# Performance work log

Measured on AMD Instinct MI355X. Metric: run time of the kernel, lower is better.

## Reference

```python
import jax, jax.numpy as jnp
import numpy as np

B, T, H, S, P, NH, NL = 16, 4096, 1024, 16, 6, 8, 2
EPS = 1e-5

def _ln(x, g, b):
    m = x.mean(-1, keepdims=True)
    v = ((x - m) ** 2).mean(-1, keepdims=True)
    return (x - m) / jnp.sqrt(v + EPS) * g + b

def _mha(q, k, v, in_w, in_b, out_w, out_b, kpm):
    dh = H // NH
    wq, wk, wv = jnp.split(in_w, 3, axis=0)
    bq, bk, bv = jnp.split(in_b, 3, axis=0)
    qh = (q @ wq.T + bq).reshape(q.shape[0], q.shape[1], NH, dh)
    kh = (k @ wk.T + bk).reshape(k.shape[0], k.shape[1], NH, dh)
    vh = (v @ wv.T + bv).reshape(v.shape[0], v.shape[1], NH, dh)
    sc = jnp.einsum('bqhd,bkhd->bhqk', qh, kh) / np.float32(np.sqrt(dh))
    if kpm is not None:
        sc = jnp.where(kpm[:, None, None, :], -1e30, sc)
    a = jax.nn.softmax(sc, axis=-1)
    o = jnp.einsum('bhqk,bkhd->bqhd', a, vh).reshape(q.shape[0], q.shape[1], H)
    return o @ out_w.T + out_b

def _segment_pool(hidden, mask):
    # vectorized ragged per-segment mean over the valid prefix of each sequence
    L = mask.sum(-1)  # [B] valid lengths (assumed >= S)
    s = jnp.arange(S + 1, dtype=jnp.float32)
    bounds = jnp.floor(s[None, :] * L[:, None].astype(jnp.float32) / S).astype(jnp.int32)  # [B,S+1]
    pos = jnp.arange(T)
    valid = pos[None, :] < L[:, None]  # [B,T]
    seg_id = (pos[None, :, None] >= bounds[:, None, 1:S]).sum(-1)  # [B,T] in [0,S-1]
    oh = ((seg_id[:, :, None] == jnp.arange(S)) & valid[:, :, None]).astype(hidden.dtype)  # [B,T,S]
    seg_sum = jnp.einsum('bts,bth->bsh', oh, hidden)
    cnt = oh.sum(1)  # [B,S]
    seg_states = seg_sum / jnp.maximum(cnt, 1.0)[..., None]
    return seg_states, cnt > 0

def setup_inputs() -> dict:
    key = jax.random.key(0)
    ks = jax.random.split(key, 32)
    p = lambda k, shp: (jax.random.normal(k, shp, jnp.float32) * 0.02)
    token_states = jax.random.normal(ks[0], (B, T, H), jnp.float32)
    lengths = jax.random.randint(ks[1], (B,), T // 2, T + 1)
    attention_mask = (jnp.arange(T)[None, :] < lengths[:, None]).astype(jnp.int32)
    inp = dict(
        token_states=token_states, attention_mask=attention_mask,
        sa_in_w=p(ks[2], (3 * H, H)), sa_in_b=jnp.zeros((3 * H,)),
        sa_out_w=p(ks[3], (H, H)), sa_out_b=jnp.zeros((H,)),
        ln_g=jnp.ones((H,)), ln_b=jnp.zeros((H,)),
        sal_w1=p(ks[4], (H, H)), sal_b1=jnp.zeros((H,)),
        sal_w2=p(ks[5], (1, H)), sal_b2=jnp.zeros((1,)),
        plan_q=p(ks[6], (P, H)),
        qa_in_w=p(ks[7], (3 * H, H)), qa_in_b=jnp.zeros((3 * H,)),
        qa_out_w=p(ks[8], (H, H)), qa_out_b=jnp.zeros((H,)),
        r_in_w=p(ks[9], (NL, 3 * H, H)), r_in_b=jnp.zeros((NL, 3 * H)),
        r_out_w=p(ks[10], (NL, H, H)), r_out_b=jnp.zeros((NL, H)),
        r_ln1_g=jnp.ones((NL, H)), r_ln1_b=jnp.zeros((NL, H)),
        r_ln2_g=jnp.ones((NL, H)), r_ln2_b=jnp.zeros((NL, H)),
        r_w1=p(ks[11], (NL, 4 * H, H)), r_b1=jnp.zeros((NL, 4 * H)),
        r_w2=p(ks[12], (NL, H, 4 * H)), r_b2=jnp.zeros((NL, H)),
    )
    return inp

def reference(token_states, attention_mask, sa_in_w, sa_in_b, sa_out_w, sa_out_b,
              ln_g, ln_b, sal_w1, sal_b1, sal_w2, sal_b2, plan_q,
              qa_in_w, qa_in_b, qa_out_w, qa_out_b,
              r_in_w, r_in_b, r_out_w, r_out_b,
              r_ln1_g, r_ln1_b, r_ln2_g, r_ln2_b, r_w1, r_b1, r_w2, r_b2):
    seg, seg_mask = _segment_pool(token_states, attention_mask)
    kpm = ~seg_mask
    attn = _mha(seg, seg, seg, sa_in_w, sa_in_b, sa_out_w, sa_out_b, kpm)
    seg = _ln(seg + attn, ln_g, ln_b)
    h = jax.nn.gelu(seg @ sal_w1.T + sal_b1, approximate=False)
    logits = (h @ sal_w2.T + sal_b2)[..., 0]
    logits = jnp.where(seg_mask, logits, -10000.0)
    sal = jax.nn.softmax(logits, axis=-1)
    wseg = seg * sal[..., None]
    query = jnp.broadcast_to(plan_q[None], (token_states.shape[0], P, H))
    plan = _mha(query, wseg, wseg, qa_in_w, qa_in_b, qa_out_w, qa_out_b, kpm)
    for l in range(NL):  # norm_first TransformerEncoder layers
        y = _ln(plan, r_ln1_g[l], r_ln1_b[l])
        plan = plan + _mha(y, y, y, r_in_w[l], r_in_b[l], r_out_w[l], r_out_b[l], None)
        y = _ln(plan, r_ln2_g[l], r_ln2_b[l])
        y = jax.nn.gelu(y @ r_w1[l].T + r_b1[l], approximate=False) @ r_w2[l].T + r_b2[l]
        plan = plan + y
    entropy = -(sal * jnp.log(sal + 1e-8)).sum(-1).mean()
    nrm = jnp.maximum(jnp.linalg.norm(plan, axis=-1, keepdims=True), 1e-12)
    npn = plan / nrm
    sim = jnp.einsum('bph,bqh->bpq', npn, npn)
    off = sim * (1.0 - jnp.eye(P, dtype=sim.dtype))
    redundancy = (off ** 2).sum() / (plan.shape[0] * P * (P - 1))
    return plan, sal, entropy, redundancy
```

## Files before the change

### kernel.cpp

```cpp
#include <hip/hip_runtime.h>
#include <hip/hip_bf16.h>
#include <math.h>

#define BB 16
#define TT 4096
#define HH 1024
#define SS 16
#define PP 6
#define NHH 8
#define DHH 128
#define NLL 2

typedef __hip_bfloat16 bf16;

__device__ __forceinline__ float b2f(bf16 x){ return __bfloat162float(x); }
__device__ __forceinline__ float us2f(unsigned short u){ return __uint_as_float(((unsigned)u) << 16); }

template<int ISBF>
__device__ __forceinline__ float ldw(const void* p, size_t i){
    if (ISBF) return b2f(((const bf16*)p)[i]);
    else      return ((const float*)p)[i];
}

__global__ void k_init(const unsigned* __restrict__ lng, float* __restrict__ scal,
                       int* __restrict__ flag){
    if (threadIdx.x == 0){
        scal[0] = 0.f; scal[1] = 0.f; scal[2] = 0.f; scal[3] = 0.f;
        flag[0] = (lng[0] == 0x3F800000u) ? 0 : 1;
    }
}

__global__ void k_len(const int* __restrict__ mask, int* __restrict__ L){
    int b = blockIdx.x, tid = threadIdx.x;
    int s = 0;
    for (int t = tid; t < TT; t += 256) s += mask[b*TT + t];
    __shared__ int red[256];
    red[tid] = s; __syncthreads();
    for (int w = 128; w > 0; w >>= 1){ if (tid < w) red[tid] += red[tid+w]; __syncthreads(); }
    if (tid == 0) L[b] = red[0];
}

template<int ISBF>
__device__ void segpool_body(const void* __restrict__ tok, const int* __restrict__ L,
                             float* __restrict__ seg){
    int s = blockIdx.x, b = blockIdx.y;
    int len = L[b];
    int lo = (s*len)/SS, hi = ((s+1)*len)/SS;
    int tid = threadIdx.x;
    int h0 = tid*4;
    float a0=0.f,a1=0.f,a2=0.f,a3=0.f;
    if (ISBF){
        const bf16* t = (const bf16*)tok;
        for (int tt = lo; tt < hi; ++tt){
            ushort4 u = *(const ushort4*)(t + ((size_t)(b*TT + tt))*HH + h0);
            a0 += us2f(u.x); a1 += us2f(u.y); a2 += us2f(u.z); a3 += us2f(u.w);
        }
    } else {
        const float* t = (const float*)tok;
        for (int tt = lo; tt < hi; ++tt){
            float4 u = *(const float4*)(t + ((size_t)(b*TT + tt))*HH + h0);
            a0 += u.x; a1 += u.y; a2 += u.z; a3 += u.w;
        }
    }
    float inv = 1.0f/(float)(hi-lo);
    float* o = seg + ((size_t)(b*SS + s))*HH + h0;
    o[0]=a0*inv; o[1]=a1*inv; o[2]=a2*inv; o[3]=a3*inv;
}
__global__ void k_segpool(const void* __restrict__ tok, const int* __restrict__ L,
                          float* __restrict__ seg, const int* __restrict__ flag){
    if (*flag) segpool_body<1>(tok, L, seg); else segpool_body<0>(tok, L, seg);
}

__global__ __launch_bounds__(256) void k_gemmsk(
        const float* __restrict__ X, const void* __restrict__ W,
        float* __restrict__ part, int N, int K, int M,
        size_t offW, int kChunk, const int* __restrict__ flag){
    __shared__ float As[16][68], Bs[16][68];
    const int tid = threadIdx.x;
    const int r0 = blockIdx.y*64, c0 = blockIdx.x*64;
    const int tx = tid & 15, ty = tid >> 4;
    const int sr = tid >> 2;
    const int sk = (tid & 3) << 2;
    const int kbeg = blockIdx.z * kChunk, kend = kbeg + kChunk;
    const int isbf = *flag;
    float c[4][4] = {{0.f,0.f,0.f,0.f},{0.f,0.f,0.f,0.f},{0.f,0.f,0.f,0.f},{0.f,0.f,0.f,0.f}};
    for (int k0 = kbeg; k0 < kend; k0 += 16){
        float4 av = make_float4(0.f,0.f,0.f,0.f);
        if (r0 + sr < N) av = *(const float4*)(X + (size_t)(r0+sr)*K + k0 + sk);
        float4 bv;
        if (isbf){
            ushort4 u = *(const ushort4*)((const bf16*)W + offW + (size_t)(c0+sr)*K + k0 + sk);
            bv = make_float4(us2f(u.x), us2f(u.y), us2f(u.z), us2f(u.w));
        } else {
            bv = *(const float4*)((const float*)W + offW + (size_t)(c0+sr)*K + k0 + sk);
        }
        As[sk+0][sr]=av.x; As[sk+1][sr]=av.y; As[sk+2][sr]=av.z; As[sk+3][sr]=av.w;
        Bs[sk+0][sr]=bv.x; Bs[sk+1][sr]=bv.y; Bs[sk+2][sr]=bv.z; Bs[sk+3][sr]=bv.w;
        __syncthreads();
        #pragma unroll
        for (int kk = 0; kk < 16; ++kk){
            float4 a = *(const float4*)&As[kk][ty<<2];
            float4 b = *(const float4*)&Bs[kk][tx<<2];
            c[0][0] += a.x*b.x; c[0][1] += a.x*b.y; c[0][2] += a.x*b.z; c[0][3] += a.x*b.w;
            c[1][0] += a.y*b.x; c[1][1] += a.y*b.y; c[1][2] += a.y*b.z; c[1][3] += a.y*b.w;
            c[2][0] += a.z*b.x; c[2][1] += a.z*b.y; c[2][2] += a.z*b.z; c[2][3] += a.z*b.w;
            c[3][0] += a.w*b.x; c[3][1] += a.w*b.y; c[3][2] += a.w*b.z; c[3][3] += a.w*b.w;
        }
        __syncthreads();
    }
    float* dst = part + (size_t)blockIdx.z * ((size_t)N * M);
    #pragma unroll
    for (int i = 0; i < 4; ++i){
        int r = r0 + (ty<<2) + i;
        if (r < N){
            float4 st = make_float4(c[i][0], c[i][1], c[i][2], c[i][3]);
            *(float4*)(dst + (size_t)r*M + c0 + (tx<<2)) = st;
        }
    }
}

template<int ACT, int RES>
__global__ void k_epi(const float* __restrict__ part, const void* __restrict__ bias,
                      const float* __restrict__ R, float* __restrict__ Y,
                      int M, int offB, int total, int SK, const int* __restrict__ flag){
    int i = blockIdx.x*256 + threadIdx.x;
    if (i >= total) return;
    float v = 0.f;
    for (int z = 0; z < SK; ++z) v += part[(size_t)z*total + i];
    int col = i % M;
    v += (*flag) ? b2f(((const bf16*)bias)[offB + col]) : ((const float*)bias)[offB + col];
    if (ACT == 1) v = 0.5f*v*(1.0f + erff(v*0.70710678118654752f));
    if (RES == 1) v += R[i];
    Y[i] = v;
}

static void gemm_sk(hipStream_t st, const float* X, const void* W, const void* bias,
                    const float* R, float* Y, float* part, const int* flag,
                    int N, int K, int M, size_t offW, int offB, int SK, int act, int res){
    dim3 g(M/64, (N+63)/64, SK);
    k_gemmsk<<<g, 256, 0, st>>>(X, W, part, N, K, M, offW, K/SK, flag);
    int total = N*M;
    int nb = (total + 255)/256;
    if (act){
        if (res) k_epi<1,1><<<nb,256,0,st>>>(part, bias, R, Y, M, offB, total, SK, flag);
        else     k_epi<1,0><<<nb,256,0,st>>>(part, bias, R, Y, M, offB, total, SK, flag);
    } else {
        if (res) k_epi<0,1><<<nb,256,0,st>>>(part, bias, R, Y, M, offB, total, SK, flag);
        else     k_epi<0,0><<<nb,256,0,st>>>(part, bias, R, Y, M, offB, total, SK, flag);
    }
}

__global__ void k_attn(const float* __restrict__ Qb, const float* __restrict__ Kb,
                       const float* __restrict__ Vb, float* __restrict__ O,
                       int nq, int nk, int sQ, int sKV, int qShared){
    __shared__ float Qs[16][DHH], Ks[16][DHH], Vs[16][DHH];
    __shared__ float sc[16][17];
    int b = blockIdx.x / NHH, h = blockIdx.x % NHH;
    int tid = threadIdx.x;
    for (int idx = tid; idx < nq*DHH; idx += 256){
        int i = idx >> 7, d = idx & 127;
        int r = qShared ? i : (b*nq + i);
        Qs[i][d] = Qb[(size_t)r*sQ + h*DHH + d];
    }
    for (int idx = tid; idx < nk*DHH; idx += 256){
        int j = idx >> 7, d = idx & 127;
        Ks[j][d] = Kb[(size_t)(b*nk + j)*sKV + h*DHH + d];
        Vs[j][d] = Vb[(size_t)(b*nk + j)*sKV + h*DHH + d];
    }
    __syncthreads();
    const float scale = 0.0883883476483184406f;
    for (int idx = tid; idx < nq*nk; idx += 256){
        int i = idx / nk, j = idx % nk;
        float s = 0.f;
        for (int d = 0; d < DHH; ++d) s += Qs[i][d]*Ks[j][d];
        sc[i][j] = s * scale;
    }
    __syncthreads();
    if (tid < nq){
        float m = -1e30f;
        for (int j = 0; j < nk; ++j) m = fmaxf(m, sc[tid][j]);
        float ssum = 0.f;
        for (int j = 0; j < nk; ++j){ float e = expf(sc[tid][j] - m); sc[tid][j] = e; ssum += e; }
        float inv = 1.0f/ssum;
        for (int j = 0; j < nk; ++j) sc[tid][j] *= inv;
    }
    __syncthreads();
    for (int idx = tid; idx < nq*DHH; idx += 256){
        int i = idx >> 7, d = idx & 127;
        float o = 0.f;
        for (int j = 0; j < nk; ++j) o += sc[i][j]*Vs[j][d];
        O[(size_t)(b*nq + i)*HH + h*DHH + d] = o;
    }
}

template<int ISBF>
__device__ void ln_body(const float* __restrict__ X, const void* __restrict__ g,
                        const void* __restrict__ bta, float* __restrict__ Y, int off){
    int row = blockIdx.x, tid = threadIdx.x;
    const float* x = X + (size_t)row*HH;
    float v[4]; float s = 0.f, sq = 0.f;
    #pragma unroll
    for (int u = 0; u < 4; ++u){ v[u] = x[tid + u*256]; s += v[u]; sq += v[u]*v[u]; }
    __shared__ float r1[256], r2[256];
    r1[tid] = s; r2[tid] = sq; __syncthreads();
    for (int w = 128; w > 0; w >>= 1){
        if (tid < w){ r1[tid] += r1[tid+w]; r2[tid] += r2[tid+w]; }
        __syncthreads();
    }
    float mean = r1[0]*(1.0f/HH);
    float var  = fmaxf(r2[0]*(1.0f/HH) - mean*mean, 0.f);
    float rstd = rsqrtf(var + 1e-5f);
    float* y = Y + (size_t)row*HH;
    #pragma unroll
    for (int u = 0; u < 4; ++u){
        int c = tid + u*256;
        y[c] = (v[u]-mean)*rstd*ldw<ISBF>(g, (size_t)(off+c)) + ldw<ISBF>(bta, (size_t)(off+c));
    }
}
__global__ void k_ln(const float* __restrict__ X, const void* __restrict__ g,
                     const void* __restrict__ bta, float* __restrict__ Y,
                     int off, const int* __restrict__ flag){
    if (*flag) ln_body<1>(X,g,bta,Y,off); else ln_body<0>(X,g,bta,Y,off);
}

template<int ISBF>
__device__ void sal_body(const float* __restrict__ Hbuf, const void* __restrict__ w2,
                         const void* __restrict__ b2v, float* __restrict__ sal,
                         float* __restrict__ scal){
    int b = blockIdx.x, tid = threadIdx.x;
    __shared__ float red[256];
    __shared__ float lg[SS];
    for (int s = 0; s < SS; ++s){
        const float* hr = Hbuf + (size_t)(b*SS + s)*HH;
        float acc = 0.f;
        for (int k = tid; k < HH; k += 256) acc += hr[k]*ldw<ISBF>(w2, (size_t)k);
        red[tid] = acc; __syncthreads();
        for (int w = 128; w > 0; w >>= 1){ if (tid < w) red[tid] += red[tid+w]; __syncthreads(); }
        if (tid == 0) lg[s] = red[0] + ldw<ISBF>(b2v, 0);
        __syncthreads();
    }
    if (tid == 0){
        float m = -1e30f;
        for (int s = 0; s < SS; ++s) m = fmaxf(m, lg[s]);
        float ssum = 0.f;
        for (int s = 0; s < SS; ++s){ float e = expf(lg[s]-m); lg[s] = e; ssum += e; }
        float inv = 1.0f/ssum, ent = 0.f;
        for (int s = 0; s < SS; ++s){
            float p = lg[s]*inv;
            sal[b*SS+s] = p;
            ent -= p*logf(p + 1e-8f);
        }
        atomicAdd(&scal[0], ent);
    }
}
__global__ void k_sal(const float* __restrict__ Hbuf, const void* __restrict__ w2,
                      const void* __restrict__ b2v, float* __restrict__ sal,
                      float* __restrict__ scal, const int* __restrict__ flag){
    if (*flag) sal_body<1>(Hbuf,w2,b2v,sal,scal); else sal_body<0>(Hbuf,w2,b2v,sal,scal);
}

__global__ void k_wseg(const float* __restrict__ seg, const float* __restrict__ sal,
                       float* __restrict__ wseg){
    int i = blockIdx.x*256 + threadIdx.x;
    wseg[i] = seg[i]*sal[i/HH];
}

__global__ void k_cvt(const void* __restrict__ in, float* __restrict__ out, int n,
                      const int* __restrict__ flag){
    int i = blockIdx.x*256 + threadIdx.x;
    if (i < n){
        if (*flag) out[i] = b2f(((const bf16*)in)[i]);
        else       out[i] = ((const float*)in)[i];
    }
}

__global__ void k_red(const float* __restrict__ plan, float* __restrict__ scal){
    int b = blockIdx.x, tid = threadIdx.x;
    __shared__ float Pl[PP][HH];
    __shared__ float red[256];
    __shared__ float nrm[PP];
    for (int idx = tid; idx < PP*HH; idx += 256)
        Pl[idx/HH][idx%HH] = plan[(size_t)b*PP*HH + idx];
    __syncthreads();
    for (int p = 0; p < PP; ++p){
        float a = 0.f;
        for (int k = tid; k < HH; k += 256){ float v = Pl[p][k]; a += v*v; }
        red[tid] = a; __syncthreads();
        for (int w = 128; w > 0; w >>= 1){ if (tid < w) red[tid] += red[tid+w]; __syncthreads(); }
        if (tid == 0) nrm[p] = fmaxf(sqrtf(red[0]), 1e-12f);
        __syncthreads();
    }
    float total = 0.f;
    for (int p = 0; p < PP; ++p){
        for (int q = p+1; q < PP; ++q){
            float a = 0.f;
            for (int k = tid; k < HH; k += 256) a += Pl[p][k]*Pl[q][k];
            red[tid] = a; __syncthreads();
            for (int w = 128; w > 0; w >>= 1){ if (tid < w) red[tid] += red[tid+w]; __syncthreads(); }
            if (tid == 0){ float s = red[0]/(nrm[p]*nrm[q]); total += 2.0f*s*s; }
            __syncthreads();
        }
    }
    if (tid == 0) atomicAdd(&scal[1], total);
}

__global__ void k_out(const float* __restrict__ plan, const float* __restrict__ sal,
                      const float* __restrict__ scal, void* __restrict__ outv,
                      const int* __restrict__ flag){
    int i = blockIdx.x*256 + threadIdx.x;
    const int NPLAN = BB*PP*HH;
    const int NSAL  = BB*SS;
    float v;
    if (i < NPLAN) v = plan[i];
    else if (i < NPLAN + NSAL) v = sal[i - NPLAN];
    else if (i == NPLAN + NSAL) v = scal[0] * (1.0f/BB);
    else if (i == NPLAN + NSAL + 1) v = scal[1] * (1.0f/(BB*PP*(PP-1)));
    else return;
    if (*flag) ((bf16*)outv)[i] = __float2bfloat16(v);
    else       ((float*)outv)[i] = v;
}

extern "C" void kernel_launch(void* const* d_in, const int* in_sizes, int n_in,
                              void* d_out, int out_size, void* d_ws, size_t ws_size,
                              hipStream_t stream) {
    const void* tok      = d_in[0];
    const int*  mask     = (const int*)d_in[1];
    const void* sa_in_w  = d_in[2];
    const void* sa_in_b  = d_in[3];
    const void* sa_out_w = d_in[4];
    const void* sa_out_b = d_in[5];
    const void* ln_g     = d_in[6];
    const void* ln_b     = d_in[7];
    const void* sal_w1   = d_in[8];
    const void* sal_b1   = d_in[9];
    const void* sal_w2   = d_in[10];
    const void* sal_b2   = d_in[11];
    const void* plan_q   = d_in[12];
    const void* qa_in_w  = d_in[13];
    const void* qa_in_b  = d_in[14];
    const void* qa_out_w = d_in[15];
    const void* qa_out_b = d_in[16];
    const void* r_in_w   = d_in[17];
    const void* r_in_b   = d_in[18];
    const void* r_out_w  = d_in[19];
    const void* r_out_b  = d_in[20];
    const void* r_ln1_g  = d_in[21];
    const void* r_ln1_b  = d_in[22];
    const void* r_ln2_g  = d_in[23];
    const void* r_ln2_b  = d_in[24];
    const void* r_w1     = d_in[25];
    const void* r_b1     = d_in[26];
    const void* r_w2     = d_in[27];
    const void* r_b2     = d_in[28];

    float* ws   = (float*)d_ws;
    float* seg  = ws;
    float* qkv  = seg  + BB*SS*HH;
    float* t1   = qkv  + BB*SS*3*HH;
    float* t2   = t1   + BB*SS*HH;
    float* plan = t2   + BB*SS*HH;
    float* ybuf = plan + BB*PP*HH;
    float* qkv2 = ybuf + BB*PP*HH;
    float* pbuf = qkv2 + BB*PP*4*HH;
    float* sal  = pbuf + BB*PP*HH;
    float* qx   = sal  + BB*SS;
    float* qh   = qx   + PP*HH;
    float* part = qh   + PP*HH;
    float* scal = part + 2*BB*SS*3*HH;
    int*   Lw   = (int*)(scal + 4);
    int*   flag = Lw + BB;

    k_init<<<1, 64, 0, stream>>>((const unsigned*)ln_g, scal, flag);
    k_len<<<BB, 256, 0, stream>>>(mask, Lw);
    k_segpool<<<dim3(SS, BB), 256, 0, stream>>>(tok, Lw, seg, flag);

    gemm_sk(stream, seg, sa_in_w, sa_in_b, nullptr, qkv, part, flag,
            BB*SS, HH, 3*HH, (size_t)0, 0, 2, 0, 0);
    k_attn<<<BB*NHH, 256, 0, stream>>>(qkv, qkv+HH, qkv+2*HH, t1, SS, SS, 3*HH, 3*HH, 0);
    gemm_sk(stream, t1, sa_out_w, sa_out_b, seg, t2, part, flag,
            BB*SS, HH, HH, (size_t)0, 0, 4, 0, 1);
    k_ln<<<BB*SS, 256, 0, stream>>>(t2, ln_g, ln_b, seg, 0, flag);

    gemm_sk(stream, seg, sal_w1, sal_b1, nullptr, t1, part, flag,
            BB*SS, HH, HH, (size_t)0, 0, 4, 1, 0);
    k_sal<<<BB, 256, 0, stream>>>(t1, sal_w2, sal_b2, sal, scal, flag);
    k_wseg<<<BB*SS*HH/256, 256, 0, stream>>>(seg, sal, t2);

    k_cvt<<<(PP*HH+255)/256, 256, 0, stream>>>(plan_q, qx, PP*HH, flag);
    gemm_sk(stream, qx, qa_in_w, qa_in_b, nullptr, qh, part, flag,
            PP, HH, HH, (size_t)0, 0, 8, 0, 0);
    gemm_sk(stream, t2, qa_in_w, qa_in_b, nullptr, qkv, part, flag,
            BB*SS, HH, 2*HH, (size_t)HH*HH, HH, 2, 0, 0);
    k_attn<<<BB*NHH, 256, 0, stream>>>(qh, qkv, qkv+HH, pbuf, PP, SS, HH, 2*HH, 1);
    gemm_sk(stream, pbuf, qa_out_w, qa_out_b, nullptr, plan, part, flag,
            BB*PP, HH, HH, (size_t)0, 0, 8, 0, 0);

    for (int l = 0; l < NLL; ++l){
        k_ln<<<BB*PP, 256, 0, stream>>>(plan, r_ln1_g, r_ln1_b, ybuf, l*HH, flag);
        gemm_sk(stream, ybuf, r_in_w, r_in_b, nullptr, qkv2, part, flag,
                BB*PP, HH, 3*HH, (size_t)l*3*HH*HH, l*3*HH, 4, 0, 0);
        k_attn<<<BB*NHH, 256, 0, stream>>>(qkv2, qkv2+HH, qkv2+2*HH, pbuf, PP, PP, 3*HH, 3*HH, 0);
        gemm_sk(stream, pbuf, r_out_w, r_out_b, plan, plan, part, flag,
                BB*PP, HH, HH, (size_t)l*HH*HH, l*HH, 8, 0, 1);
        k_ln<<<BB*PP, 256, 0, stream>>>(plan, r_ln2_g, r_ln2_b, ybuf, l*HH, flag);
        gemm_sk(stream, ybuf, r_w1, r_b1, nullptr, qkv2, part, flag,
                BB*PP, HH, 4*HH, (size_t)l*4*HH*HH, l*4*HH, 2, 1, 0);
        gemm_sk(stream, qkv2, r_w2, r_b2, plan, plan, part, flag,
                BB*PP, 4*HH, HH, (size_t)l*HH*4*HH, l*HH, 8, 0, 1);
    }

    k_red<<<BB, 256, 0, stream>>>(plan, scal);
    k_out<<<(BB*PP*HH + BB*SS + 2 + 255)/256, 256, 0, stream>>>(plan, sal, scal, d_out, flag);
}
```

Measured before the change: 1.039 ms.

## Rewrite pipeline with bf16 MFMA GEMMs, split-precision activations, fused LN and segpool

Replaces the FP32 split-K SIMT GEMMs and their separate epilogue kernels with bf16 MFMA GEMMs. Activations are split into hi/lo bf16 pairs to keep near-fp32 accuracy, and bias, GELU and residual are fused into the GEMM epilogue. Output projections are fused with the following LayerNorm. The length, init and segment-pool kernels are merged into one wider pooling kernel, and the dtype flag is read inline. This cuts launch count, partial-sum traffic and scalar FMA work, at the cost of extra shadow buffers and doubled MFMA count for the lo parts.

```diff
diff --git a/kernel.cpp b/kernel.cpp
--- a/kernel.cpp
+++ b/kernel.cpp
@@ -12,312 +12,608 @@
 #define NLL 2
 
 typedef __hip_bfloat16 bf16;
+typedef __attribute__((ext_vector_type(8))) short s8v;
+typedef __attribute__((ext_vector_type(4))) float f32x4;
+#define MFMA_B16(a,b,c) __builtin_amdgcn_mfma_f32_16x16x32_bf16((a),(b),(c),0,0,0)
 
 __device__ __forceinline__ float b2f(bf16 x){ return __bfloat162float(x); }
 __device__ __forceinline__ float us2f(unsigned short u){ return __uint_as_float(((unsigned)u) << 16); }
-
+__device__ __forceinline__ int is_bf(const unsigned* lng){ return lng[0]==0x3F800000u ? 0 : 1; }
+__device__ __forceinline__ float geluf(float v){ return 0.5f*v*(1.0f+erff(v*0.70710678118654752f)); }
+
+__device__ __forceinline__ void split_bf(float x, ushort& h, ushort& l){
+    unsigned xb = __float_as_uint(x);
+    unsigned hh = (xb + 0x7FFFu + ((xb>>16)&1u)) >> 16;
+    float hf = __uint_as_float(hh<<16);
+    float r = x - hf;
+    unsigned rb = __float_as_uint(r);
+    unsigned ll = (rb + 0x7FFFu + ((rb>>16)&1u)) >> 16;
+    h=(ushort)hh; l=(ushort)ll;
+}
 template<int ISBF>
 __device__ __forceinline__ float ldw(const void* p, size_t i){
     if (ISBF) return b2f(((const bf16*)p)[i]);
     else      return ((const float*)p)[i];
 }
 
-__global__ void k_init(const unsigned* __restrict__ lng, float* __restrict__ scal,
-                       int* __restrict__ flag){
-    if (threadIdx.x == 0){
-        scal[0] = 0.f; scal[1] = 0.f; scal[2] = 0.f; scal[3] = 0.f;
-        flag[0] = (lng[0] == 0x3F800000u) ? 0 : 1;
-    }
-}
-
-__global__ void k_len(const int* __restrict__ mask, int* __restrict__ L){
-    int b = blockIdx.x, tid = threadIdx.x;
-    int s = 0;
-    for (int t = tid; t < TT; t += 256) s += mask[b*TT + t];
-    __shared__ int red[256];
-    red[tid] = s; __syncthreads();
-    for (int w = 128; w > 0; w >>= 1){ if (tid < w) red[tid] += red[tid+w]; __syncthreads(); }
-    if (tid == 0) L[b] = red[0];
-}
-
-template<int ISBF>
-__device__ void segpool_body(const void* __restrict__ tok, const int* __restrict__ L,
-                             float* __restrict__ seg){
-    int s = blockIdx.x, b = blockIdx.y;
-    int len = L[b];
-    int lo = (s*len)/SS, hi = ((s+1)*len)/SS;
-    int tid = threadIdx.x;
-    int h0 = tid*4;
-    float a0=0.f,a1=0.f,a2=0.f,a3=0.f;
-    if (ISBF){
-        const bf16* t = (const bf16*)tok;
-        for (int tt = lo; tt < hi; ++tt){
-            ushort4 u = *(const ushort4*)(t + ((size_t)(b*TT + tt))*HH + h0);
-            a0 += us2f(u.x); a1 += us2f(u.y); a2 += us2f(u.z); a3 += us2f(u.w);
+__global__ __launch_bounds__(1024) void k_segpool(const void* __restrict__ tok,
+        const int* __restrict__ mask, float* __restrict__ seg,
+        ushort* __restrict__ sh, ushort* __restrict__ sl,
+        float* __restrict__ scal, const unsigned* __restrict__ lng){
+    __shared__ float sm[8*1024];
+    int s = blockIdx.x, b = blockIdx.y, tid = threadIdx.x;
+    if (s==0 && b==0 && tid==0){ scal[0]=0.f; scal[1]=0.f; scal[2]=0.f; scal[3]=0.f; }
+    int* smi = (int*)sm;
+    int a0i = 0;
+    #pragma unroll
+    for (int u=0;u<4;++u) a0i += mask[b*TT + tid + u*1024];
+    smi[tid]=a0i; __syncthreads();
+    for (int w=512;w>0;w>>=1){ if (tid<w) smi[tid]+=smi[tid+w]; __syncthreads(); }
+    int len = smi[0];
+    __syncthreads();
+    int lo=(s*len)/SS, hi=((s+1)*len)/SS;
+    float inv = 1.0f/(float)(hi-lo);
+    if (is_bf(lng)){
+        int ro = tid >> 7;
+        int c8 = (tid & 127) << 3;
+        float a[8];
+        #pragma unroll
+        for (int i=0;i<8;++i) a[i]=0.f;
+        const unsigned short* t = (const unsigned short*)tok;
+        for (int tt = lo + ro; tt < hi; tt += 8){
+            uint4 u = *(const uint4*)(t + ((size_t)(b*TT + tt))*HH + c8);
+            a[0]+=us2f((unsigned short)(u.x&0xffff)); a[1]+=us2f((unsigned short)(u.x>>16));
+            a[2]+=us2f((unsigned short)(u.y&0xffff)); a[3]+=us2f((unsigned short)(u.y>>16));
+            a[4]+=us2f((unsigned short)(u.z&0xffff)); a[5]+=us2f((unsigned short)(u.z>>16));
+            a[6]+=us2f((unsigned short)(u.w&0xffff)); a[7]+=us2f((unsigned short)(u.w>>16));
+        }
+        #pragma unroll
+        for (int i=0;i<8;++i) sm[ro*1024 + c8 + i] = a[i];
+        __syncthreads();
+        if (ro == 0){
+            #pragma unroll
+            for (int r=1;r<8;++r)
+                #pragma unroll
+                for (int i=0;i<8;++i) a[i] += sm[r*1024 + c8 + i];
+            size_t base = ((size_t)(b*SS + s))*HH + c8;
+            #pragma unroll
+            for (int i=0;i<8;++i){
+                float v = a[i]*inv;
+                seg[base+i] = v;
+                ushort h_,l_; split_bf(v,h_,l_);
+                sh[base+i]=h_; sl[base+i]=l_;
+            }
         }
     } else {
+        int ro = tid >> 8;
+        int c4 = (tid & 255) << 2;
+        float a[4] = {0.f,0.f,0.f,0.f};
         const float* t = (const float*)tok;
-        for (int tt = lo; tt < hi; ++tt){
-            float4 u = *(const float4*)(t + ((size_t)(b*TT + tt))*HH + h0);
-            a0 += u.x; a1 += u.y; a2 += u.z; a3 += u.w;
-        }
-    }
-    float inv = 1.0f/(float)(hi-lo);
-    float* o = seg + ((size_t)(b*SS + s))*HH + h0;
-    o[0]=a0*inv; o[1]=a1*inv; o[2]=a2*inv; o[3]=a3*inv;
-}
-__global__ void k_segpool(const void* __restrict__ tok, const int* __restrict__ L,
-                          float* __restrict__ seg, const int* __restrict__ flag){
-    if (*flag) segpool_body<1>(tok, L, seg); else segpool_body<0>(tok, L, seg);
-}
-
-__global__ __launch_bounds__(256) void k_gemmsk(
-        const float* __restrict__ X, const void* __restrict__ W,
-        float* __restrict__ part, int N, int K, int M,
-        size_t offW, int kChunk, const int* __restrict__ flag){
+        for (int tt = lo + ro; tt < hi; tt += 4){
+            float4 u = *(const float4*)(t + ((size_t)(b*TT + tt))*HH + c4);
+            a[0]+=u.x; a[1]+=u.y; a[2]+=u.z; a[3]+=u.w;
+        }
+        #pragma unroll
+        for (int i=0;i<4;++i) sm[ro*1024 + c4 + i] = a[i];
+        __syncthreads();
+        if (ro == 0){
+            #pragma unroll
+            for (int r=1;r<4;++r)
+                #pragma unroll
+                for (int i=0;i<4;++i) a[i] += sm[r*1024 + c4 + i];
+            size_t base = ((size_t)(b*SS + s))*HH + c4;
+            #pragma unroll
+            for (int i=0;i<4;++i) seg[base+i] = a[i]*inv;
+        }
+    }
+}
+
+template<int ACT,int RES,int SHAD,int RAWA>
+__global__ __launch_bounds__(256) void k_gemm_t(
+        const float* __restrict__ Xf, const ushort* __restrict__ Ah, const ushort* __restrict__ Al,
+        const void* __restrict__ W, const void* __restrict__ bias, const float* __restrict__ Rres,
+        float* __restrict__ Y, ushort* __restrict__ Yh, ushort* __restrict__ Yl,
+        int N, int K, int M, size_t offW, int offB, const unsigned* __restrict__ lng){
     __shared__ float As[16][68], Bs[16][68];
     const int tid = threadIdx.x;
-    const int r0 = blockIdx.y*64, c0 = blockIdx.x*64;
-    const int tx = tid & 15, ty = tid >> 4;
-    const int sr = tid >> 2;
-    const int sk = (tid & 3) << 2;
-    const int kbeg = blockIdx.z * kChunk, kend = kbeg + kChunk;
-    const int isbf = *flag;
-    float c[4][4] = {{0.f,0.f,0.f,0.f},{0.f,0.f,0.f,0.f},{0.f,0.f,0.f,0.f},{0.f,0.f,0.f,0.f}};
-    for (int k0 = kbeg; k0 < kend; k0 += 16){
-        float4 av = make_float4(0.f,0.f,0.f,0.f);
-        if (r0 + sr < N) av = *(const float4*)(X + (size_t)(r0+sr)*K + k0 + sk);
-        float4 bv;
-        if (isbf){
-            ushort4 u = *(const ushort4*)((const bf16*)W + offW + (size_t)(c0+sr)*K + k0 + sk);
-            bv = make_float4(us2f(u.x), us2f(u.y), us2f(u.z), us2f(u.w));
-        } else {
-            bv = *(const float4*)((const float*)W + offW + (size_t)(c0+sr)*K + k0 + sk);
-        }
-        As[sk+0][sr]=av.x; As[sk+1][sr]=av.y; As[sk+2][sr]=av.z; As[sk+3][sr]=av.w;
-        Bs[sk+0][sr]=bv.x; Bs[sk+1][sr]=bv.y; Bs[sk+2][sr]=bv.z; Bs[sk+3][sr]=bv.w;
-        __syncthreads();
-        #pragma unroll
-        for (int kk = 0; kk < 16; ++kk){
-            float4 a = *(const float4*)&As[kk][ty<<2];
-            float4 b = *(const float4*)&Bs[kk][tx<<2];
-            c[0][0] += a.x*b.x; c[0][1] += a.x*b.y; c[0][2] += a.x*b.z; c[0][3] += a.x*b.w;
-            c[1][0] += a.y*b.x; c[1][1] += a.y*b.y; c[1][2] += a.y*b.z; c[1][3] += a.y*b.w;
-            c[2][0] += a.z*b.x; c[2][1] += a.z*b.y; c[2][2] += a.z*b.z; c[2][3] += a.z*b.w;
-            c[3][0] += a.w*b.x; c[3][1] += a.w*b.y; c[3][2] += a.w*b.z; c[3][3] += a.w*b.w;
-        }
-        __syncthreads();
-    }
-    float* dst = part + (size_t)blockIdx.z * ((size_t)N * M);
-    #pragma unroll
-    for (int i = 0; i < 4; ++i){
-        int r = r0 + (ty<<2) + i;
-        if (r < N){
-            float4 st = make_float4(c[i][0], c[i][1], c[i][2], c[i][3]);
-            *(float4*)(dst + (size_t)r*M + c0 + (tx<<2)) = st;
-        }
-    }
-}
-
-template<int ACT, int RES>
-__global__ void k_epi(const float* __restrict__ part, const void* __restrict__ bias,
-                      const float* __restrict__ R, float* __restrict__ Y,
-                      int M, int offB, int total, int SK, const int* __restrict__ flag){
-    int i = blockIdx.x*256 + threadIdx.x;
-    if (i >= total) return;
-    float v = 0.f;
-    for (int z = 0; z < SK; ++z) v += part[(size_t)z*total + i];
-    int col = i % M;
-    v += (*flag) ? b2f(((const bf16*)bias)[offB + col]) : ((const float*)bias)[offB + col];
-    if (ACT == 1) v = 0.5f*v*(1.0f + erff(v*0.70710678118654752f));
-    if (RES == 1) v += R[i];
-    Y[i] = v;
-}
-
-static void gemm_sk(hipStream_t st, const float* X, const void* W, const void* bias,
-                    const float* R, float* Y, float* part, const int* flag,
-                    int N, int K, int M, size_t offW, int offB, int SK, int act, int res){
-    dim3 g(M/64, (N+63)/64, SK);
-    k_gemmsk<<<g, 256, 0, st>>>(X, W, part, N, K, M, offW, K/SK, flag);
-    int total = N*M;
-    int nb = (total + 255)/256;
-    if (act){
-        if (res) k_epi<1,1><<<nb,256,0,st>>>(part, bias, R, Y, M, offB, total, SK, flag);
-        else     k_epi<1,0><<<nb,256,0,st>>>(part, bias, R, Y, M, offB, total, SK, flag);
+    const int c0 = blockIdx.x*64;
+    if (is_bf(lng)){
+        const int l=tid&63, wv=tid>>6, lr=l&15, lk=(l>>4)<<3;
+        const int r0 = blockIdx.y*64 + wv*16;
+        int ar = r0 + lr; if (ar > N-1) ar = N-1;
+        const ushort* pah = Ah + (size_t)ar*K + lk;
+        const ushort* pal = nullptr;
+        if (!RAWA) pal = Al + (size_t)ar*K + lk;
+        const ushort* pw = (const ushort*)W + offW + (size_t)(c0+lr)*K + lk;
+        const size_t w16 = (size_t)16*K;
+        f32x4 a0={0.f,0.f,0.f,0.f}, a1={0.f,0.f,0.f,0.f};
+        f32x4 a2={0.f,0.f,0.f,0.f}, a3={0.f,0.f,0.f,0.f};
+        for (int k=0;k<K;k+=32){
+            s8v ah = *(const s8v*)pah;
+            s8v b0 = *(const s8v*)pw;
+            s8v b1 = *(const s8v*)(pw + w16);
+            s8v b2 = *(const s8v*)(pw + 2*w16);
+            s8v b3 = *(const s8v*)(pw + 3*w16);
+            a0=MFMA_B16(ah,b0,a0); a1=MFMA_B16(ah,b1,a1);
+            a2=MFMA_B16(ah,b2,a2); a3=MFMA_B16(ah,b3,a3);
+            if (!RAWA){
+                s8v al_ = *(const s8v*)pal;
+                a0=MFMA_B16(al_,b0,a0); a1=MFMA_B16(al_,b1,a1);
+                a2=MFMA_B16(al_,b2,a2); a3=MFMA_B16(al_,b3,a3);
+                pal += 32;
+            }
+            pah += 32; pw += 32;
+        }
+        const int rb = r0 + ((l>>4)<<2);
+        #pragma unroll
+        for (int rg=0;rg<4;++rg){
+            int r = rb+rg;
+            if (r < N){
+                float vv[4] = {a0[rg],a1[rg],a2[rg],a3[rg]};
+                #pragma unroll
+                for (int j=0;j<4;++j){
+                    int col = c0 + j*16 + lr;
+                    float v = vv[j] + ldw<1>(bias,(size_t)(offB+col));
+                    if (ACT) v = geluf(v);
+                    if (RES) v += Rres[(size_t)r*M+col];
+                    Y[(size_t)r*M+col] = v;
+                    if (SHAD){ ushort h_,l_; split_bf(v,h_,l_);
+                        Yh[(size_t)r*M+col]=h_; Yl[(size_t)r*M+col]=l_; }
+                }
+            }
+        }
     } else {
-        if (res) k_epi<0,1><<<nb,256,0,st>>>(part, bias, R, Y, M, offB, total, SK, flag);
-        else     k_epi<0,0><<<nb,256,0,st>>>(part, bias, R, Y, M, offB, total, SK, flag);
-    }
-}
-
-__global__ void k_attn(const float* __restrict__ Qb, const float* __restrict__ Kb,
+        const int r0 = blockIdx.y*64;
+        const int tx = tid&15, ty = tid>>4, sr = tid>>2, sk = (tid&3)<<2;
+        float c4[4][4] = {{0.f,0.f,0.f,0.f},{0.f,0.f,0.f,0.f},{0.f,0.f,0.f,0.f},{0.f,0.f,0.f,0.f}};
+        const float* Xs = RAWA ? Xf : Xf;
+        for (int k0=0;k0<K;k0+=16){
+            float4 av = make_float4(0.f,0.f,0.f,0.f);
+            if (r0+sr < N) av = *(const float4*)(Xs + (size_t)(r0+sr)*K + k0 + sk);
+            float4 bv = *(const float4*)((const float*)W + offW + (size_t)(c0+sr)*K + k0 + sk);
+            As[sk+0][sr]=av.x; As[sk+1][sr]=av.y; As[sk+2][sr]=av.z; As[sk+3][sr]=av.w;
+            Bs[sk+0][sr]=bv.x; Bs[sk+1][sr]=bv.y; Bs[sk+2][sr]=bv.z; Bs[sk+3][sr]=bv.w;
+            __syncthreads();
+            #pragma unroll
+            for (int kk=0;kk<16;++kk){
+                float4 a = *(const float4*)&As[kk][ty<<2];
+                float4 b = *(const float4*)&Bs[kk][tx<<2];
+                c4[0][0]+=a.x*b.x; c4[0][1]+=a.x*b.y; c4[0][2]+=a.x*b.z; c4[0][3]+=a.x*b.w;
+                c4[1][0]+=a.y*b.x; c4[1][1]+=a.y*b.y; c4[1][2]+=a.y*b.z; c4[1][3]+=a.y*b.w;
+                c4[2][0]+=a.z*b.x; c4[2][1]+=a.z*b.y; c4[2][2]+=a.z*b.z; c4[2][3]+=a.z*b.w;
+                c4[3][0]+=a.w*b.x; c4[3][1]+=a.w*b.y; c4[3][2]+=a.w*b.z; c4[3][3]+=a.w*b.w;
+            }
+            __syncthreads();
+        }
+        #pragma unroll
+        for (int i=0;i<4;++i){
+            int r = r0 + (ty<<2) + i;
+            if (r < N){
+                #pragma unroll
+                for (int j=0;j<4;++j){
+                    int col = c0 + (tx<<2) + j;
+                    float v = c4[i][j] + ((const float*)bias)[offB+col];
+                    if (ACT) v = geluf(v);
+                    if (RES) v += Rres[(size_t)r*M+col];
+                    Y[(size_t)r*M+col] = v;
+                }
+            }
+        }
+    }
+}
+
+template<int RES,int HASY>
+__global__ __launch_bounds__(512) void k_rowln(
+        const float* __restrict__ Xf, const ushort* __restrict__ Ah, const ushort* __restrict__ Al,
+        const void* __restrict__ W, const void* __restrict__ bias, const float* __restrict__ Rres,
+        float* __restrict__ Y, float* __restrict__ Z, ushort* __restrict__ Zh, ushort* __restrict__ Zl,
+        const void* __restrict__ g, const void* __restrict__ bta,
+        size_t offW, int offB, int lnoff, const unsigned* __restrict__ lng){
+    __shared__ float smx[8256+320];
+    float* As  = smx;
+    float* smS = smx + 8256;
+    float* smQ = smS + 128;
+    float* smM = smQ + 128;
+    float* smR = smM + 16;
+    const int tid = threadIdx.x;
+    const int r0 = blockIdx.x*16;
+    if (is_bf(lng)){
+        const int w=tid>>6, l=tid&63, lr=l&15, lk=(l>>4)<<3, g4=l>>4;
+        const ushort* pah = Ah + (size_t)(r0+lr)*HH + lk;
+        const ushort* pal = Al + (size_t)(r0+lr)*HH + lk;
+        const int cbase = w*128;
+        const ushort* wp = (const ushort*)W + offW + (size_t)(cbase+lr)*HH + lk;
+        const size_t w16 = (size_t)16*HH;
+        f32x4 acc[8];
+        #pragma unroll
+        for (int s=0;s<8;++s) acc[s] = (f32x4){0.f,0.f,0.f,0.f};
+        for (int k=0;k<HH;k+=32){
+            s8v ah = *(const s8v*)pah;
+            s8v al_ = *(const s8v*)pal;
+            #pragma unroll
+            for (int s=0;s<8;++s){
+                s8v bv = *(const s8v*)(wp + (size_t)s*w16);
+                acc[s]=MFMA_B16(ah,bv,acc[s]);
+                acc[s]=MFMA_B16(al_,bv,acc[s]);
+            }
+            pah+=32; pal+=32; wp+=32;
+        }
+        float ps[4]={0.f,0.f,0.f,0.f}, pq[4]={0.f,0.f,0.f,0.f};
+        #pragma unroll
+        for (int s=0;s<8;++s){
+            int col = cbase + s*16 + lr;
+            float bv = ldw<1>(bias,(size_t)(offB+col));
+            #pragma unroll
+            for (int rg=0;rg<4;++rg){
+                int r = r0 + g4*4 + rg;
+                float v = acc[s][rg] + bv;
+                if (RES)  v += Rres[(size_t)r*HH+col];
+                if (HASY) Y[(size_t)r*HH+col] = v;
+                acc[s][rg] = v;
+                ps[rg]+=v; pq[rg]+=v*v;
+            }
+        }
+        #pragma unroll
+        for (int m=1;m<16;m<<=1){
+            #pragma unroll
+            for (int rg=0;rg<4;++rg){
+                ps[rg]+=__shfl_xor(ps[rg],m);
+                pq[rg]+=__shfl_xor(pq[rg],m);
+            }
+        }
+        if (lr==0){
+            #pragma unroll
+            for (int rg=0;rg<4;++rg){ smS[w*16+g4*4+rg]=ps[rg]; smQ[w*16+g4*4+rg]=pq[rg]; }
+        }
+        __syncthreads();
+        if (tid<16){
+            float S=0.f,Q=0.f;
+            #pragma unroll
+            for (int ww=0;ww<8;++ww){ S+=smS[ww*16+tid]; Q+=smQ[ww*16+tid]; }
+            float mean=S*(1.0f/HH);
+            float var=fmaxf(Q*(1.0f/HH)-mean*mean,0.f);
+            smM[tid]=mean; smR[tid]=rsqrtf(var+1e-5f);
+        }
+        __syncthreads();
+        #pragma unroll
+        for (int s=0;s<8;++s){
+            int col = cbase + s*16 + lr;
+            float gg = ldw<1>(g,(size_t)(lnoff+col));
+            float bb = ldw<1>(bta,(size_t)(lnoff+col));
+            #pragma unroll
+            for (int rg=0;rg<4;++rg){
+                int r = r0 + g4*4 + rg;
+                float zv = (acc[s][rg]-smM[g4*4+rg])*smR[g4*4+rg]*gg+bb;
+                Z[(size_t)r*HH+col]=zv;
+                ushort h_,l_; split_bf(zv,h_,l_);
+                Zh[(size_t)r*HH+col]=h_; Zl[(size_t)r*HH+col]=l_;
+            }
+        }
+    } else {
+        float acc0[16], acc1[16];
+        #pragma unroll
+        for (int r=0;r<16;++r){ acc0[r]=0.f; acc1[r]=0.f; }
+        const float* Wf = (const float*)W;
+        for (int ko=0;ko<HH;ko+=512){
+            for (int i=tid;i<16*512;i+=512){ int rr=i>>9, cc=i&511; As[rr*516+cc]=Xf[(size_t)(r0+rr)*HH+ko+cc]; }
+            __syncthreads();
+            const float* wp0 = Wf + offW + (size_t)tid*HH + ko;
+            const float* wp1 = Wf + offW + (size_t)(tid+512)*HH + ko;
+            for (int k=0;k<512;++k){
+                float wa=wp0[k], wb=wp1[k];
+                #pragma unroll
+                for (int r=0;r<16;++r){ float av=As[r*516+k]; acc0[r]+=av*wa; acc1[r]+=av*wb; }
+            }
+            __syncthreads();
+        }
+        const float* bf_ = (const float*)bias;
+        float b0=bf_[offB+tid], b1v=bf_[offB+tid+512];
+        float s16[16], q16[16];
+        #pragma unroll
+        for (int r=0;r<16;++r){
+            float v0=acc0[r]+b0, v1=acc1[r]+b1v;
+            if (RES){ v0+=Rres[(size_t)(r0+r)*HH+tid]; v1+=Rres[(size_t)(r0+r)*HH+tid+512]; }
+            if (HASY){ Y[(size_t)(r0+r)*HH+tid]=v0; Y[(size_t)(r0+r)*HH+tid+512]=v1; }
+            acc0[r]=v0; acc1[r]=v1;
+            s16[r]=v0+v1; q16[r]=v0*v0+v1*v1;
+        }
+        #pragma unroll
+        for (int m=1;m<64;m<<=1){
+            #pragma unroll
+            for (int r=0;r<16;++r){ s16[r]+=__shfl_xor(s16[r],m); q16[r]+=__shfl_xor(q16[r],m); }
+        }
+        int w=tid>>6, l=tid&63;
+        if (l==0){
+            #pragma unroll
+            for (int r=0;r<16;++r){ smS[w*16+r]=s16[r]; smQ[w*16+r]=q16[r]; }
+        }
+        __syncthreads();
+        if (tid<16){
+            float S=0.f,Q=0.f;
+            #pragma unroll
+            for (int ww=0;ww<8;++ww){ S+=smS[ww*16+tid]; Q+=smQ[ww*16+tid]; }
+            float mean=S*(1.0f/HH);
+            float var=fmaxf(Q*(1.0f/HH)-mean*mean,0.f);
+            smM[tid]=mean; smR[tid]=rsqrtf(var+1e-5f);
+        }
+        __syncthreads();
+        const float* gf=(const float*)g; const float* btf=(const float*)bta;
+        float g0=gf[lnoff+tid], g1=gf[lnoff+tid+512];
+        float t0=btf[lnoff+tid], t1v=btf[lnoff+tid+512];
+        #pragma unroll
+        for (int r=0;r<16;++r){
+            Z[(size_t)(r0+r)*HH+tid]     =(acc0[r]-smM[r])*smR[r]*g0+t0;
+            Z[(size_t)(r0+r)*HH+tid+512] =(acc1[r]-smM[r])*smR[r]*g1+t1v;
+        }
+    }
+}
+
+__global__ __launch_bounds__(512) void k_sal(
+        const float* __restrict__ segF, const ushort* __restrict__ segH, const ushort* __restrict__ segL,
+        const void* __restrict__ w1, const void* __restrict__ b1,
+        const void* __restrict__ w2, const void* __restrict__ b2v,
+        float* __restrict__ sal, float* __restrict__ t2, ushort* __restrict__ t2h, ushort* __restrict__ t2l,
+        float* __restrict__ scal, const unsigned* __restrict__ lng){
+    __shared__ float smx[8256+320];
+    float* As  = smx;
+    float* smS = smx + 8256;
+    float* lgv = smS + 128;
+    float* salv= lgv + 16;
+    const int tid = threadIdx.x, b = blockIdx.x;
+    const int r0 = b*16;
+    const int bfm = is_bf(lng);
+    if (bfm){
+        const int w=tid>>6, l=tid&63, lr=l&15, lk=(l>>4)<<3, g4=l>>4;
+        const ushort* pah = segH + (size_t)(r0+lr)*HH + lk;
+        const ushort* pal = segL + (size_t)(r0+lr)*HH + lk;
+        const int cbase = w*128;
+        const ushort* wp = (const ushort*)w1 + (size_t)(cbase+lr)*HH + lk;
+        const size_t w16 = (size_t)16*HH;
+        f32x4 acc[8];
+        #pragma unroll
+        for (int s=0;s<8;++s) acc[s] = (f32x4){0.f,0.f,0.f,0.f};
+        for (int k=0;k<HH;k+=32){
+            s8v ah = *(const s8v*)pah;
+            s8v al_ = *(const s8v*)pal;
+            #pragma unroll
+            for (int s=0;s<8;++s){
+                s8v bv = *(const s8v*)(wp + (size_t)s*w16);
+                acc[s]=MFMA_B16(ah,bv,acc[s]);
+                acc[s]=MFMA_B16(al_,bv,acc[s]);
+            }
+            pah+=32; pal+=32; wp+=32;
+        }
+        float ls[4]={0.f,0.f,0.f,0.f};
+        #pragma unroll
+        for (int s=0;s<8;++s){
+            int col = cbase + s*16 + lr;
+            float bb = ldw<1>(b1,(size_t)col);
+            float w2v = ldw<1>(w2,(size_t)col);
+            #pragma unroll
+            for (int rg=0;rg<4;++rg) ls[rg] += geluf(acc[s][rg]+bb)*w2v;
+        }
+        #pragma unroll
+        for (int m=1;m<16;m<<=1){
+            #pragma unroll
+            for (int rg=0;rg<4;++rg) ls[rg]+=__shfl_xor(ls[rg],m);
+        }
+        if (lr==0){
+            #pragma unroll
+            for (int rg=0;rg<4;++rg) smS[w*16+g4*4+rg]=ls[rg];
+        }
+        __syncthreads();
+        if (tid<16){
+            float S=0.f;
+            #pragma unroll
+            for (int ww=0;ww<8;++ww) S+=smS[ww*16+tid];
+            lgv[tid]=S+ldw<1>(b2v,0);
+        }
+        __syncthreads();
+    } else {
+        float acc0[16], acc1[16];
+        #pragma unroll
+        for (int r=0;r<16;++r){ acc0[r]=0.f; acc1[r]=0.f; }
+        const float* w1f=(const float*)w1;
+        for (int ko=0;ko<HH;ko+=512){
+            for (int i=tid;i<16*512;i+=512){ int rr=i>>9, cc=i&511; As[rr*516+cc]=segF[(size_t)(r0+rr)*HH+ko+cc]; }
+            __syncthreads();
+            const float* wp0 = w1f + (size_t)tid*HH + ko;
+            const float* wp1 = w1f + (size_t)(tid+512)*HH + ko;
+            for (int k=0;k<512;++k){
+                float wa=wp0[k], wb=wp1[k];
+                #pragma unroll
+                for (int r=0;r<16;++r){ float av=As[r*516+k]; acc0[r]+=av*wa; acc1[r]+=av*wb; }
+            }
+            __syncthreads();
+        }
+        const float* b1f=(const float*)b1; const float* w2f=(const float*)w2;
+        float ba=b1f[tid], bb=b1f[tid+512];
+        float wa2=w2f[tid], wb2=w2f[tid+512];
+        float ls[16];
+        #pragma unroll
+        for (int r=0;r<16;++r)
+            ls[r]=geluf(acc0[r]+ba)*wa2 + geluf(acc1[r]+bb)*wb2;
+        #pragma unroll
+        for (int m=1;m<64;m<<=1){
+            #pragma unroll
+            for (int r=0;r<16;++r) ls[r]+=__shfl_xor(ls[r],m);
+        }
+        int w=tid>>6, l=tid&63;
+        if (l==0){
+            #pragma unroll
+            for (int r=0;r<16;++r) smS[w*16+r]=ls[r];
+        }
+        __syncthreads();
+        if (tid<16){
+            float S=0.f;
+            #pragma unroll
+            for (int ww=0;ww<8;++ww) S+=smS[ww*16+tid];
+            lgv[tid]=S+((const float*)b2v)[0];
+        }
+        __syncthreads();
+    }
+    if (tid==0){
+        float m=-1e30f;
+        for (int s2=0;s2<SS;++s2) m=fmaxf(m,lgv[s2]);
+        float ev[SS]; float ssum=0.f;
+        for (int s2=0;s2<SS;++s2){ ev[s2]=expf(lgv[s2]-m); ssum+=ev[s2]; }
+        float inv2=1.0f/ssum, ent=0.f;
+        for (int s2=0;s2<SS;++s2){
+            float p=ev[s2]*inv2;
+            salv[s2]=p; sal[b*SS+s2]=p;
+            ent-=p*logf(p+1e-8f);
+        }
+        atomicAdd(&scal[0], ent);
+    }
+    __syncthreads();
+    for (int i=tid;i<SS*HH;i+=512){
+        int rr=i>>10;
+        float v = segF[(size_t)r0*HH + i] * salv[rr];
+        size_t oi=(size_t)r0*HH + i;
+        t2[oi]=v;
+        if (bfm){ ushort h_,l_; split_bf(v,h_,l_); t2h[oi]=h_; t2l[oi]=l_; }
+    }
+}
+
+__global__ __launch_bounds__(256) void k_attn(const float* __restrict__ Qb, const float* __restrict__ Kb,
                        const float* __restrict__ Vb, float* __restrict__ O,
-                       int nq, int nk, int sQ, int sKV, int qShared){
-    __shared__ float Qs[16][DHH], Ks[16][DHH], Vs[16][DHH];
+                       ushort* __restrict__ Oh, ushort* __restrict__ Ol,
+                       int nq, int nk, int sQ, int sKV, int qShared,
+                       const unsigned* __restrict__ lng){
+    __shared__ float Qs[16][132], Ks[16][132], Vs[16][132];
     __shared__ float sc[16][17];
     int b = blockIdx.x / NHH, h = blockIdx.x % NHH;
     int tid = threadIdx.x;
-    for (int idx = tid; idx < nq*DHH; idx += 256){
-        int i = idx >> 7, d = idx & 127;
-        int r = qShared ? i : (b*nq + i);
-        Qs[i][d] = Qb[(size_t)r*sQ + h*DHH + d];
-    }
-    for (int idx = tid; idx < nk*DHH; idx += 256){
-        int j = idx >> 7, d = idx & 127;
-        Ks[j][d] = Kb[(size_t)(b*nk + j)*sKV + h*DHH + d];
-        Vs[j][d] = Vb[(size_t)(b*nk + j)*sKV + h*DHH + d];
+    int bfm = is_bf(lng);
+    for (int idx=tid; idx<nq*32; idx+=256){
+        int i = idx>>5, d4=(idx&31)<<2;
+        int r = qShared ? i : (b*nq+i);
+        *(float4*)&Qs[i][d4] = *(const float4*)&Qb[(size_t)r*sQ + h*DHH + d4];
+    }
+    for (int idx=tid; idx<nk*32; idx+=256){
+        int j=idx>>5, d4=(idx&31)<<2;
+        *(float4*)&Ks[j][d4] = *(const float4*)&Kb[(size_t)(b*nk+j)*sKV + h*DHH + d4];
+        *(float4*)&Vs[j][d4] = *(const float4*)&Vb[(size_t)(b*nk+j)*sKV + h*DHH + d4];
     }
     __syncthreads();
     const float scale = 0.0883883476483184406f;
-    for (int idx = tid; idx < nq*nk; idx += 256){
-        int i = idx / nk, j = idx % nk;
-        float s = 0.f;
-        for (int d = 0; d < DHH; ++d) s += Qs[i][d]*Ks[j][d];
-        sc[i][j] = s * scale;
+    for (int idx=tid; idx<nq*nk; idx+=256){
+        int i=idx/nk, j=idx-i*nk;
+        const float4* qp=(const float4*)&Qs[i][0];
+        const float4* kp=(const float4*)&Ks[j][0];
+        float ax=0.f,ay=0.f,az=0.f,aw=0.f;
+        #pragma unroll
+        for (int k4=0;k4<32;++k4){
+            float4 a=qp[k4], c=kp[k4];
+            ax+=a.x*c.x; ay+=a.y*c.y; az+=a.z*c.z; aw+=a.w*c.w;
+        }
+        sc[i][j]=(ax+ay+az+aw)*scale;
     }
     __syncthreads();
-    if (tid < nq){
-        float m = -1e30f;
-        for (int j = 0; j < nk; ++j) m = fmaxf(m, sc[tid][j]);
-        float ssum = 0.f;
-        for (int j = 0; j < nk; ++j){ float e = expf(sc[tid][j] - m); sc[tid][j] = e; ssum += e; }
-        float inv = 1.0f/ssum;
-        for (int j = 0; j < nk; ++j) sc[tid][j] *= inv;
+    if (tid<nq){
+        float m=-1e30f;
+        for (int j=0;j<nk;++j) m=fmaxf(m,sc[tid][j]);
+        float ssum=0.f;
+        for (int j=0;j<nk;++j){ float e=expf(sc[tid][j]-m); sc[tid][j]=e; ssum+=e; }
+        float inv=1.0f/ssum;
+        for (int j=0;j<nk;++j) sc[tid][j]*=inv;
     }
     __syncthreads();
-    for (int idx = tid; idx < nq*DHH; idx += 256){
-        int i = idx >> 7, d = idx & 127;
-        float o = 0.f;
-        for (int j = 0; j < nk; ++j) o += sc[i][j]*Vs[j][d];
-        O[(size_t)(b*nq + i)*HH + h*DHH + d] = o;
-    }
-}
-
-template<int ISBF>
-__device__ void ln_body(const float* __restrict__ X, const void* __restrict__ g,
-                        const void* __restrict__ bta, float* __restrict__ Y, int off){
-    int row = blockIdx.x, tid = threadIdx.x;
+    for (int idx=tid; idx<nq*32; idx+=256){
+        int i=idx>>5, d4=(idx&31)<<2;
+        float ox=0.f,oy=0.f,oz=0.f,ow=0.f;
+        for (int j=0;j<nk;++j){
+            float s=sc[i][j];
+            float4 v=*(const float4*)&Vs[j][d4];
+            ox+=s*v.x; oy+=s*v.y; oz+=s*v.z; ow+=s*v.w;
+        }
+        size_t oidx=(size_t)(b*nq+i)*HH + h*DHH + d4;
+        *(float4*)&O[oidx]=make_float4(ox,oy,oz,ow);
+        if (bfm){
+            ushort4 hv,lv;
+            split_bf(ox,hv.x,lv.x); split_bf(oy,hv.y,lv.y);
+            split_bf(oz,hv.z,lv.z); split_bf(ow,hv.w,lv.w);
+            *(ushort4*)&Oh[oidx]=hv; *(ushort4*)&Ol[oidx]=lv;
+        }
+    }
+}
+
+__global__ __launch_bounds__(256) void k_ln(const float* __restrict__ X, const void* __restrict__ g,
+        const void* __restrict__ bta, float* __restrict__ Z,
+        ushort* __restrict__ Zh, ushort* __restrict__ Zl, int off,
+        const unsigned* __restrict__ lng){
+    int row=blockIdx.x, tid=threadIdx.x;
     const float* x = X + (size_t)row*HH;
-    float v[4]; float s = 0.f, sq = 0.f;
+    float v[4]; float s=0.f, sq=0.f;
     #pragma unroll
-    for (int u = 0; u < 4; ++u){ v[u] = x[tid + u*256]; s += v[u]; sq += v[u]*v[u]; }
+    for (int u=0;u<4;++u){ v[u]=x[tid+u*256]; s+=v[u]; sq+=v[u]*v[u]; }
     __shared__ float r1[256], r2[256];
-    r1[tid] = s; r2[tid] = sq; __syncthreads();
-    for (int w = 128; w > 0; w >>= 1){
-        if (tid < w){ r1[tid] += r1[tid+w]; r2[tid] += r2[tid+w]; }
-        __syncthreads();
-    }
-    float mean = r1[0]*(1.0f/HH);
-    float var  = fmaxf(r2[0]*(1.0f/HH) - mean*mean, 0.f);
-    float rstd = rsqrtf(var + 1e-5f);
-    float* y = Y + (size_t)row*HH;
+    r1[tid]=s; r2[tid]=sq; __syncthreads();
+    for (int w=128;w>0;w>>=1){
+        if (tid<w){ r1[tid]+=r1[tid+w]; r2[tid]+=r2[tid+w]; }
+        __syncthreads();
+    }
+    float mean=r1[0]*(1.0f/HH);
+    float var=fmaxf(r2[0]*(1.0f/HH)-mean*mean,0.f);
+    float rstd=rsqrtf(var+1e-5f);
+    int bfm = is_bf(lng);
     #pragma unroll
-    for (int u = 0; u < 4; ++u){
-        int c = tid + u*256;
-        y[c] = (v[u]-mean)*rstd*ldw<ISBF>(g, (size_t)(off+c)) + ldw<ISBF>(bta, (size_t)(off+c));
-    }
-}
-__global__ void k_ln(const float* __restrict__ X, const void* __restrict__ g,
-                     const void* __restrict__ bta, float* __restrict__ Y,
-                     int off, const int* __restrict__ flag){
-    if (*flag) ln_body<1>(X,g,bta,Y,off); else ln_body<0>(X,g,bta,Y,off);
-}
-
-template<int ISBF>
-__device__ void sal_body(const float* __restrict__ Hbuf, const void* __restrict__ w2,
-                         const void* __restrict__ b2v, float* __restrict__ sal,
-                         float* __restrict__ scal){
-    int b = blockIdx.x, tid = threadIdx.x;
-    __shared__ float red[256];
-    __shared__ float lg[SS];
-    for (int s = 0; s < SS; ++s){
-        const float* hr = Hbuf + (size_t)(b*SS + s)*HH;
-        float acc = 0.f;
-        for (int k = tid; k < HH; k += 256) acc += hr[k]*ldw<ISBF>(w2, (size_t)k);
-        red[tid] = acc; __syncthreads();
-        for (int w = 128; w > 0; w >>= 1){ if (tid < w) red[tid] += red[tid+w]; __syncthreads(); }
-        if (tid == 0) lg[s] = red[0] + ldw<ISBF>(b2v, 0);
-        __syncthreads();
-    }
-    if (tid == 0){
-        float m = -1e30f;
-        for (int s = 0; s < SS; ++s) m = fmaxf(m, lg[s]);
-        float ssum = 0.f;
-        for (int s = 0; s < SS; ++s){ float e = expf(lg[s]-m); lg[s] = e; ssum += e; }
-        float inv = 1.0f/ssum, ent = 0.f;
-        for (int s = 0; s < SS; ++s){
-            float p = lg[s]*inv;
-            sal[b*SS+s] = p;
-            ent -= p*logf(p + 1e-8f);
-        }
-        atomicAdd(&scal[0], ent);
-    }
-}
-__global__ void k_sal(const float* __restrict__ Hbuf, const void* __restrict__ w2,
-                      const void* __restrict__ b2v, float* __restrict__ sal,
-                      float* __restrict__ scal, const int* __restrict__ flag){
-    if (*flag) sal_body<1>(Hbuf,w2,b2v,sal,scal); else sal_body<0>(Hbuf,w2,b2v,sal,scal);
-}
-
-__global__ void k_wseg(const float* __restrict__ seg, const float* __restrict__ sal,
-                       float* __restrict__ wseg){
-    int i = blockIdx.x*256 + threadIdx.x;
-    wseg[i] = seg[i]*sal[i/HH];
-}
-
-__global__ void k_cvt(const void* __restrict__ in, float* __restrict__ out, int n,
-                      const int* __restrict__ flag){
-    int i = blockIdx.x*256 + threadIdx.x;
-    if (i < n){
-        if (*flag) out[i] = b2f(((const bf16*)in)[i]);
-        else       out[i] = ((const float*)in)[i];
-    }
-}
-
-__global__ void k_red(const float* __restrict__ plan, float* __restrict__ scal){
-    int b = blockIdx.x, tid = threadIdx.x;
+    for (int u=0;u<4;++u){
+        int c=tid+u*256;
+        float gv = bfm ? b2f(((const bf16*)g)[off+c])   : ((const float*)g)[off+c];
+        float bv = bfm ? b2f(((const bf16*)bta)[off+c]) : ((const float*)bta)[off+c];
+        float zv=(v[u]-mean)*rstd*gv+bv;
+        Z[(size_t)row*HH+c]=zv;
+        if (bfm){ ushort h_,l_; split_bf(zv,h_,l_);
+            Zh[(size_t)row*HH+c]=h_; Zl[(size_t)row*HH+c]=l_; }
+    }
+}
+
+__global__ __launch_bounds__(256) void k_red(const float* __restrict__ plan, float* __restrict__ scal){
     __shared__ float Pl[PP][HH];
     __shared__ float red[256];
-    __shared__ float nrm[PP];
-    for (int idx = tid; idx < PP*HH; idx += 256)
-        Pl[idx/HH][idx%HH] = plan[(size_t)b*PP*HH + idx];
+    __shared__ float dv[21];
+    int b=blockIdx.x, tid=threadIdx.x;
+    for (int i=tid;i<PP*HH;i+=256) Pl[i>>10][i&1023]=plan[(size_t)b*PP*HH+i];
     __syncthreads();
-    for (int p = 0; p < PP; ++p){
-        float a = 0.f;
-        for (int k = tid; k < HH; k += 256){ float v = Pl[p][k]; a += v*v; }
-        red[tid] = a; __syncthreads();
-        for (int w = 128; w > 0; w >>= 1){ if (tid < w) red[tid] += red[tid+w]; __syncthreads(); }
-        if (tid == 0) nrm[p] = fmaxf(sqrtf(red[0]), 1e-12f);
-        __syncthreads();
-    }
-    float total = 0.f;
-    for (int p = 0; p < PP; ++p){
-        for (int q = p+1; q < PP; ++q){
-            float a = 0.f;
-            for (int k = tid; k < HH; k += 256) a += Pl[p][k]*Pl[q][k];
-            red[tid] = a; __syncthreads();
-            for (int w = 128; w > 0; w >>= 1){ if (tid < w) red[tid] += red[tid+w]; __syncthreads(); }
-            if (tid == 0){ float s = red[0]/(nrm[p]*nrm[q]); total += 2.0f*s*s; }
-            __syncthreads();
-        }
-    }
-    if (tid == 0) atomicAdd(&scal[1], total);
-}
-
-__global__ void k_out(const float* __restrict__ plan, const float* __restrict__ sal,
+    const int PRa[21]={0,1,2,3,4,5, 0,0,0,0,0,1,1,1,1,2,2,2,3,3,4};
+    const int QRa[21]={0,1,2,3,4,5, 1,2,3,4,5,2,3,4,5,3,4,5,4,5,5};
+    for (int t=0;t<21;++t){
+        float a=0.f;
+        #pragma unroll
+        for (int u=0;u<4;++u){ int c=tid+u*256; a+=Pl[PRa[t]][c]*Pl[QRa[t]][c]; }
+        red[tid]=a; __syncthreads();
+        for (int w=128;w>0;w>>=1){ if (tid<w) red[tid]+=red[tid+w]; __syncthreads(); }
+        if (tid==0) dv[t]=red[0];
+        __syncthreads();
+    }
+    if (tid==0){
+        float n[PP];
+        #pragma unroll
+        for (int p=0;p<PP;++p) n[p]=fmaxf(sqrtf(dv[p]),1e-12f);
+        float tot=0.f;
+        for (int k=6;k<21;++k){
+            float s=dv[k]/(n[PRa[k]]*n[QRa[k]]);
+            tot+=2.0f*s*s;
+        }
+        atomicAdd(&scal[1], tot);
+    }
+}
+
+__global__ __launch_bounds__(256) void k_out(const float* __restrict__ plan, const float* __restrict__ sal,
                       const float* __restrict__ scal, void* __restrict__ outv,
-                      const int* __restrict__ flag){
+                      const unsigned* __restrict__ lng){
     int i = blockIdx.x*256 + threadIdx.x;
     const int NPLAN = BB*PP*HH;
     const int NSAL  = BB*SS;
     float v;
     if (i < NPLAN) v = plan[i];
-    else if (i < NPLAN + NSAL) v = sal[i - NPLAN];
-    else if (i == NPLAN + NSAL) v = scal[0] * (1.0f/BB);
-    else if (i == NPLAN + NSAL + 1) v = scal[1] * (1.0f/(BB*PP*(PP-1)));
+    else if (i < NPLAN+NSAL) v = sal[i-NPLAN];
+    else if (i == NPLAN+NSAL) v = scal[0]*(1.0f/BB);
+    else if (i == NPLAN+NSAL+1) v = scal[1]*(1.0f/(BB*PP*(PP-1)));
     else return;
-    if (*flag) ((bf16*)outv)[i] = __float2bfloat16(v);
-    else       ((float*)outv)[i] = v;
+    if (is_bf(lng)) ((bf16*)outv)[i]=__float2bfloat16(v);
+    else            ((float*)outv)[i]=v;
 }
 
 extern "C" void kernel_launch(void* const* d_in, const int* in_sizes, int n_in,
@@ -352,6 +648,7 @@
     const void* r_b1     = d_in[26];
     const void* r_w2     = d_in[27];
     const void* r_b2     = d_in[28];
+    const unsigned* lng  = (const unsigned*)ln_g;
 
     float* ws   = (float*)d_ws;
     float* seg  = ws;
@@ -362,53 +659,55 @@
     float* ybuf = plan + BB*PP*HH;
     float* qkv2 = ybuf + BB*PP*HH;
     float* pbuf = qkv2 + BB*PP*4*HH;
-    float* sal  = pbuf + BB*PP*HH;
-    float* qx   = sal  + BB*SS;
-    float* qh   = qx   + PP*HH;
-    float* part = qh   + PP*HH;
-    float* scal = part + 2*BB*SS*3*HH;
-    int*   Lw   = (int*)(scal + 4);
-    int*   flag = Lw + BB;
-
-    k_init<<<1, 64, 0, stream>>>((const unsigned*)ln_g, scal, flag);
-    k_len<<<BB, 256, 0, stream>>>(mask, Lw);
-    k_segpool<<<dim3(SS, BB), 256, 0, stream>>>(tok, Lw, seg, flag);
-
-    gemm_sk(stream, seg, sa_in_w, sa_in_b, nullptr, qkv, part, flag,
-            BB*SS, HH, 3*HH, (size_t)0, 0, 2, 0, 0);
-    k_attn<<<BB*NHH, 256, 0, stream>>>(qkv, qkv+HH, qkv+2*HH, t1, SS, SS, 3*HH, 3*HH, 0);
-    gemm_sk(stream, t1, sa_out_w, sa_out_b, seg, t2, part, flag,
-            BB*SS, HH, HH, (size_t)0, 0, 4, 0, 1);
-    k_ln<<<BB*SS, 256, 0, stream>>>(t2, ln_g, ln_b, seg, 0, flag);
-
-    gemm_sk(stream, seg, sal_w1, sal_b1, nullptr, t1, part, flag,
-            BB*SS, HH, HH, (size_t)0, 0, 4, 1, 0);
-    k_sal<<<BB, 256, 0, stream>>>(t1, sal_w2, sal_b2, sal, scal, flag);
-    k_wseg<<<BB*SS*HH/256, 256, 0, stream>>>(seg, sal, t2);
-
-    k_cvt<<<(PP*HH+255)/256, 256, 0, stream>>>(plan_q, qx, PP*HH, flag);
-    gemm_sk(stream, qx, qa_in_w, qa_in_b, nullptr, qh, part, flag,
-            PP, HH, HH, (size_t)0, 0, 8, 0, 0);
-    gemm_sk(stream, t2, qa_in_w, qa_in_b, nullptr, qkv, part, flag,
-            BB*SS, HH, 2*HH, (size_t)HH*HH, HH, 2, 0, 0);
-    k_attn<<<BB*NHH, 256, 0, stream>>>(qh, qkv, qkv+HH, pbuf, PP, SS, HH, 2*HH, 1);
-    gemm_sk(stream, pbuf, qa_out_w, qa_out_b, nullptr, plan, part, flag,
-            BB*PP, HH, HH, (size_t)0, 0, 8, 0, 0);
-
-    for (int l = 0; l < NLL; ++l){
-        k_ln<<<BB*PP, 256, 0, stream>>>(plan, r_ln1_g, r_ln1_b, ybuf, l*HH, flag);
-        gemm_sk(stream, ybuf, r_in_w, r_in_b, nullptr, qkv2, part, flag,
-                BB*PP, HH, 3*HH, (size_t)l*3*HH*HH, l*3*HH, 4, 0, 0);
-        k_attn<<<BB*NHH, 256, 0, stream>>>(qkv2, qkv2+HH, qkv2+2*HH, pbuf, PP, PP, 3*HH, 3*HH, 0);
-        gemm_sk(stream, pbuf, r_out_w, r_out_b, plan, plan, part, flag,
-                BB*PP, HH, HH, (size_t)l*HH*HH, l*HH, 8, 0, 1);
-        k_ln<<<BB*PP, 256, 0, stream>>>(plan, r_ln2_g, r_ln2_b, ybuf, l*HH, flag);
-        gemm_sk(stream, ybuf, r_w1, r_b1, nullptr, qkv2, part, flag,
-                BB*PP, HH, 4*HH, (size_t)l*4*HH*HH, l*4*HH, 2, 1, 0);
-        gemm_sk(stream, qkv2, r_w2, r_b2, plan, plan, part, flag,
-                BB*PP, 4*HH, HH, (size_t)l*HH*4*HH, l*HH, 8, 0, 1);
-    }
-
-    k_red<<<BB, 256, 0, stream>>>(plan, scal);
-    k_out<<<(BB*PP*HH + BB*SS + 2 + 255)/256, 256, 0, stream>>>(plan, sal, scal, d_out, flag);
-}
+    float* qh   = pbuf + BB*PP*HH;
+    float* sal  = qh   + 16*HH;
+    ushort* segh = (ushort*)(sal + BB*SS);
+    ushort* segl = segh + BB*SS*HH;
+    ushort* t1h  = segl + BB*SS*HH;
+    ushort* t1l  = t1h  + BB*SS*HH;
+    ushort* t2h  = t1l  + BB*SS*HH;
+    ushort* t2l  = t2h  + BB*SS*HH;
+    ushort* pbh  = t2l  + BB*SS*HH;
+    ushort* pbl  = pbh  + BB*PP*HH;
+    ushort* ybh  = pbl  + BB*PP*HH;
+    ushort* ybl  = ybh  + BB*PP*HH;
+    ushort* ffh  = ybl  + BB*PP*HH;
+    ushort* ffl  = ffh  + BB*PP*4*HH;
+    float*  scal = (float*)(ffl + BB*PP*4*HH);
+
+    k_segpool<<<dim3(SS,BB),1024,0,stream>>>(tok, mask, seg, segh, segl, scal, lng);
+
+    k_gemm_t<0,0,0,0><<<dim3(48,4),256,0,stream>>>(seg, segh, segl, sa_in_w, sa_in_b, nullptr,
+        qkv, nullptr, nullptr, BB*SS, HH, 3*HH, (size_t)0, 0, lng);
+    k_attn<<<BB*NHH,256,0,stream>>>(qkv, qkv+HH, qkv+2*HH, t1, t1h, t1l, SS, SS, 3*HH, 3*HH, 0, lng);
+    k_rowln<1,0><<<16,512,0,stream>>>(t1, t1h, t1l, sa_out_w, sa_out_b, seg,
+        nullptr, seg, segh, segl, ln_g, ln_b, (size_t)0, 0, 0, lng);
+
+    k_sal<<<BB,512,0,stream>>>(seg, segh, segl, sal_w1, sal_b1, sal_w2, sal_b2,
+        sal, t2, t2h, t2l, scal, lng);
+
+    k_gemm_t<0,0,0,1><<<dim3(16,1),256,0,stream>>>((const float*)plan_q, (const ushort*)plan_q, nullptr,
+        qa_in_w, qa_in_b, nullptr, qh, nullptr, nullptr, PP, HH, HH, (size_t)0, 0, lng);
+    k_gemm_t<0,0,0,0><<<dim3(32,4),256,0,stream>>>(t2, t2h, t2l, qa_in_w, qa_in_b, nullptr,
+        qkv, nullptr, nullptr, BB*SS, HH, 2*HH, (size_t)HH*HH, HH, lng);
+    k_attn<<<BB*NHH,256,0,stream>>>(qh, qkv, qkv+HH, pbuf, pbh, pbl, PP, SS, HH, 2*HH, 1, lng);
+    k_rowln<0,1><<<6,512,0,stream>>>(pbuf, pbh, pbl, qa_out_w, qa_out_b, nullptr,
+        plan, ybuf, ybh, ybl, r_ln1_g, r_ln1_b, (size_t)0, 0, 0, lng);
+
+    for (int l=0;l<NLL;++l){
+        k_gemm_t<0,0,0,0><<<dim3(48,2),256,0,stream>>>(ybuf, ybh, ybl, r_in_w, r_in_b, nullptr,
+            qkv2, nullptr, nullptr, BB*PP, HH, 3*HH, (size_t)l*3*HH*HH, l*3*HH, lng);
+        k_attn<<<BB*NHH,256,0,stream>>>(qkv2, qkv2+HH, qkv2+2*HH, pbuf, pbh, pbl, PP, PP, 3*HH, 3*HH, 0, lng);
+        k_rowln<1,1><<<6,512,0,stream>>>(pbuf, pbh, pbl, r_out_w, r_out_b, plan,
+            plan, ybuf, ybh, ybl, r_ln2_g, r_ln2_b, (size_t)l*HH*HH, l*HH, l*HH, lng);
+        k_gemm_t<1,0,1,0><<<dim3(64,2),256,0,stream>>>(ybuf, ybh, ybl, r_w1, r_b1, nullptr,
+            qkv2, ffh, ffl, BB*PP, HH, 4*HH, (size_t)l*4*HH*HH, l*4*HH, lng);
+        k_gemm_t<0,1,0,0><<<dim3(16,2),256,0,stream>>>(qkv2, ffh, ffl, r_w2, r_b2, plan,
+            plan, nullptr, nullptr, BB*PP, 4*HH, HH, (size_t)l*HH*4*HH, l*HH, lng);
+        if (l < NLL-1)
+            k_ln<<<BB*PP,256,0,stream>>>(plan, r_ln1_g, r_ln1_b, ybuf, ybh, ybl, (l+1)*HH, lng);
+    }
+
+    k_red<<<BB,256,0,stream>>>(plan, scal);
+    k_out<<<(BB*PP*HH + BB*SS + 2 + 255)/256,256,0,stream>>>(plan, sal, scal, d_out, lng);
+}
```

Result: slower. 2.724 ms (+162.2%).
